# Performance work log

Hardware: AMD Instinct MI355X
Metric: run time of the kernel (lower is better)

The kernel has to match this reference:

```python
import jax, jax.numpy as jnp
import numpy as np


def setup_inputs() -> dict:
    key = jax.random.key(0)
    k1, k2 = jax.random.split(key)
    B, N, M, D = 8, 8192, 8192, 3
    gts = jax.random.normal(k1, (B, N, D), dtype=jnp.float32)
    preds = jax.random.normal(k2, (B, M, D), dtype=jnp.float32)
    return {"gts": gts, "preds": preds}


def reference(gts, preds):
    # Chamfer distance (pytorch3d defaults): squared L2, mean over points,
    # mean over batch, sum of both directions.
    x2 = jnp.sum(gts * gts, axis=-1)          # [B, N]
    y2 = jnp.sum(preds * preds, axis=-1)      # [B, M]
    xy = jnp.einsum('bnd,bmd->bnm', gts, preds)  # [B, N, M]
    d2 = x2[:, :, None] + y2[:, None, :] - 2.0 * xy
    d2 = jnp.maximum(d2, 0.0)  # guard tiny negative values from cancellation
    cham_x = jnp.mean(jnp.min(d2, axis=2))  # x -> nearest y, mean over N then B
    cham_y = jnp.mean(jnp.min(d2, axis=1))  # y -> nearest x, mean over M then B
    return cham_x + cham_y
```

## Files before the change

kernel.cpp:

```cpp
#include <hip/hip_runtime.h>
#include <hip/hip_bf16.h>
#include <math.h>


#define BLOCK 256
#define WAVES 4
#define QPW 64
#define NCHUNK 2
#define SREF 512
#define STAGE_BYTES (SREF * 32)
#define IPS (SREF / 64)

typedef short short8 __attribute__((ext_vector_type(8)));
typedef float f32x16 __attribute__((ext_vector_type(16)));
typedef unsigned int u32;
typedef __attribute__((address_space(1))) const u32 gu32;
typedef __attribute__((address_space(3))) u32 lu32;

__device__ __forceinline__ unsigned int bf16hi(float f) {
    __hip_bfloat16 h = __float2bfloat16(f);
    return (unsigned int)*reinterpret_cast<unsigned short*>(&h);
}
__device__ __forceinline__ float bf16f(unsigned int u) {
    unsigned short us = (unsigned short)u;
    __hip_bfloat16 h;
    *reinterpret_cast<unsigned short*>(&h) = us;
    return __bfloat162float(h);
}

__device__ __forceinline__ f32x16 mfma_bf16_z(short8 a, short8 b) {
    f32x16 d;
    asm volatile("v_mfma_f32_32x32x16_bf16 %0, %1, %2, 0"
                 : "=&v"(d) : "v"(a), "v"(b));
    return d;
}
__device__ __forceinline__ void mfma_fence4(f32x16& a, f32x16& b, f32x16& c, f32x16& d) {
    asm volatile("s_nop 7\n\ts_nop 7" : "+v"(a), "+v"(b), "+v"(c), "+v"(d));
}

__device__ __forceinline__ void gload_lds16(const void* g, void* l) {
    __builtin_amdgcn_global_load_lds((gu32*)g, (lu32*)l, 16, 0, 0);
}

__global__ void prep_kernel(const float* __restrict__ gts, const float* __restrict__ preds,
                            int nG, int nP, uint4* __restrict__ recQ,
                            unsigned char* __restrict__ recB, float* __restrict__ q2,
                            float* out) {
    const int idx = blockIdx.x * blockDim.x + threadIdx.x;
    if (idx == 0) out[0] = 0.0f;
    if (idx >= nG + nP) return;
    const float* src;
    unsigned char* rb;
    if (idx < nG) {
        src = gts + 3 * (size_t)idx;
        rb  = recB + (size_t)(idx >> 5) * 1024 + (size_t)(idx & 31) * 16;
    } else {
        const int j = idx - nG;
        src = preds + 3 * (size_t)j;
        rb  = recB + (size_t)nG * 32 + (size_t)(j >> 5) * 1024 + (size_t)(j & 31) * 16;
    }
    const float x = src[0], y = src[1], z = src[2];
    const float n2 = x * x + y * y + z * z;
    const float w = -0.5f * n2;
    q2[idx] = n2;
    const unsigned int xh = bf16hi(x), yh = bf16hi(y), zh = bf16hi(z), wh = bf16hi(w);
    const unsigned int xl = bf16hi(x - bf16f(xh));
    const unsigned int yl = bf16hi(y - bf16f(yh));
    const unsigned int zl = bf16hi(z - bf16f(zh));
    const unsigned int wl = bf16hi(w - bf16f(wh));
    const unsigned int hx = xh | (yh << 16), hz = zh | (wh << 16);
    const unsigned int lx = xl | (yl << 16), lz = zl | (wl << 16);
    recQ[idx] = make_uint4(hx, hz, lx, lz);
    *(uint4*)(rb)       = make_uint4(hx, hz, hx, hz);
    *(uint4*)(rb + 512) = make_uint4(lx, lz, 0u, 0u);
}

__global__ void __launch_bounds__(BLOCK, 4)
nn_kernel(const uint4* __restrict__ recQ, const unsigned char* __restrict__ recB,
          float* __restrict__ kpart, int N, int M, int B) {
    const int z = blockIdx.z;
    const bool dirX = (z < B);
    const int b = dirX ? z : z - B;
    const int NQ = dirX ? N : M;
    const int NR = dirX ? M : N;
    const uint4* Qr = recQ + (dirX ? 0 : (size_t)B * N) + (size_t)b * NQ;
    const int chunk = NR / NCHUNK;
    const unsigned char* Rb = recB + (dirX ? (size_t)B * N * 32 : 0)
                              + ((size_t)b * NR + (size_t)blockIdx.y * chunk) * 32;
    const int nGP = B * (N + M);
    float* outK = kpart + (size_t)blockIdx.y * nGP + (dirX ? 0 : B * N) + (size_t)b * NQ;

    const int tid = threadIdx.x;
    const int lane = tid & 63;
    const int wave = tid >> 6;
    const int m = lane & 31;
    const unsigned int loMask = (lane >= 32) ? 0u : 0xFFFFFFFFu;
    const int qBase = (blockIdx.x * WAVES + wave) * QPW;

    const uint4 q0 = Qr[qBase + m];
    const uint4 q1 = Qr[qBase + 32 + m];
    union { uint4 v; short8 s; } a;
    a.v.x = q0.x;
    a.v.y = (q0.y & 0xFFFFu) | 0x3F800000u;
    a.v.z = q0.z & loMask;
    a.v.w = q0.w & 0xFFFFu & loMask;
    const short8 A0 = a.s;
    a.v.x = q1.x;
    a.v.y = (q1.y & 0xFFFFu) | 0x3F800000u;
    a.v.z = q1.z & loMask;
    a.v.w = q1.w & 0xFFFFu & loMask;
    const short8 A1 = a.s;

    f32x16 k0, k1;
    #pragma unroll
    for (int r = 0; r < 16; ++r) { k0[r] = -INFINITY; k1[r] = -INFINITY; }

    __shared__ __align__(16) unsigned char smem[WAVES * 64 * 36 * 4];

    const unsigned char* gsrc = Rb + (size_t)wave * 4096 + (size_t)lane * 16;
    unsigned char* lbase = smem + wave * 4096;
    auto stage_issue = [&](int s) {
        const unsigned char* g = gsrc + (size_t)s * STAGE_BYTES;
        unsigned char* l = lbase + ((s & 1) * STAGE_BYTES);
        #pragma unroll
        for (int k2 = 0; k2 < 4; ++k2)
            gload_lds16(g + k2 * 1024, l + k2 * 1024);
    };

    const int nStages = chunk / SREF;
    stage_issue(0);
    __syncthreads();

    #pragma unroll 1
    for (int s = 0; s < nStages; ++s) {
        if (s + 1 < nStages) stage_issue(s + 1);
        const unsigned char* tb = smem + ((s & 1) * STAGE_BYTES) + lane * 16;
        #pragma unroll
        for (int i = 0; i < IPS; ++i) {
            const short8 b0 = *(const short8*)(tb + i * 2048);
            const short8 b1 = *(const short8*)(tb + i * 2048 + 1024);

            f32x16 c0 = mfma_bf16_z(A0, b0);
            f32x16 c1 = mfma_bf16_z(A0, b1);
            f32x16 c2 = mfma_bf16_z(A1, b0);
            f32x16 c3 = mfma_bf16_z(A1, b1);
            mfma_fence4(c0, c1, c2, c3);
            #pragma unroll
            for (int r = 0; r < 16; ++r)
                k0[r] = fmaxf(fmaxf(c0[r], c1[r]), k0[r]);
            #pragma unroll
            for (int r = 0; r < 16; ++r)
                k1[r] = fmaxf(fmaxf(c2[r], c3[r]), k1[r]);
        }
        __syncthreads();
    }

    float (*sT)[64][36] = (float (*)[64][36])smem;
    #pragma unroll
    for (int r = 0; r < 16; ++r) {
        const int row = (r & 3) + 8 * (r >> 2) + 4 * (lane >> 5);
        sT[wave][row][m]      = k0[r];
        sT[wave][32 + row][m] = k1[r];
    }
    const float4* rowp = (const float4*)&sT[wave][lane][0];
    float4 m01 = rowp[0];
    #pragma unroll
    for (int kk = 1; kk < 8; ++kk) {
        const float4 t = rowp[kk];
        m01.x = fmaxf(m01.x, t.x); m01.y = fmaxf(m01.y, t.y);
        m01.z = fmaxf(m01.z, t.z); m01.w = fmaxf(m01.w, t.w);
    }
    const float cmax = fmaxf(fmaxf(m01.x, m01.y), fmaxf(m01.z, m01.w));
    outK[qBase + lane] = cmax;
}

__global__ void __launch_bounds__(BLOCK)
reduce_kernel(const float* __restrict__ kpart, const float* __restrict__ q2,
              int nG, int nP, float invx, float invy, float* __restrict__ out) {
    const int total = nG + nP;
    float local = 0.0f;
    for (int idx = blockIdx.x * blockDim.x + threadIdx.x; idx < total;
         idx += gridDim.x * blockDim.x) {
        const float c = fmaxf(kpart[idx], kpart[total + idx]);
        const float inv = (idx < nG) ? invx : invy;
        local += fmaxf(q2[idx] - 2.0f * c, 0.0f) * inv;
    }
    __shared__ float waveSums[BLOCK / 64];
    float v = local;
    #pragma unroll
    for (int off = 32; off; off >>= 1) v += __shfl_xor(v, off);
    if ((threadIdx.x & 63) == 0) waveSums[threadIdx.x >> 6] = v;
    __syncthreads();
    if (threadIdx.x == 0) {
        float s = 0.0f;
        #pragma unroll
        for (int w = 0; w < BLOCK / 64; ++w) s += waveSums[w];
        atomicAdd(out, s);
    }
}

extern "C" void kernel_launch(void* const* d_in, const int* in_sizes, int n_in,
                              void* d_out, int out_size, void* d_ws, size_t ws_size,
                              hipStream_t stream) {
    const float* gts   = (const float*)d_in[0];
    const float* preds = (const float*)d_in[1];
    float* out = (float*)d_out;

    const int B = 8;
    const int N = in_sizes[0] / (B * 3);
    const int M = in_sizes[1] / (B * 3);
    const int nG = B * N, nP = B * M;

    uint4* recQ = (uint4*)d_ws;
    unsigned char* recB = (unsigned char*)(recQ + nG + nP);
    float* kpart = (float*)(recB + (size_t)(nG + nP) * 32);
    float* q2    = kpart + (size_t)NCHUNK * (nG + nP);

    prep_kernel<<<(nG + nP + BLOCK - 1) / BLOCK, BLOCK, 0, stream>>>(
        gts, preds, nG, nP, recQ, recB, q2, out);

    dim3 grid(N / (WAVES * QPW), NCHUNK, 2 * B);
    nn_kernel<<<grid, BLOCK, 0, stream>>>(recQ, recB, kpart, N, M, B);

    reduce_kernel<<<256, BLOCK, 0, stream>>>(
        kpart, q2, nG, nP, 1.0f / (float)nG, 1.0f / (float)nP, out);
}
```

Measured before the change: 99.49 us.

## Software-pipeline MFMA with max-folding using double-buffered accumulator sets

Result: no change. 98.17 us (-1.3%).

```diff
diff --git a/kernel.cpp b/kernel.cpp
--- a/kernel.cpp
+++ b/kernel.cpp
@@ -17,6 +17,8 @@
 typedef __attribute__((address_space(1))) const u32 gu32;
 typedef __attribute__((address_space(3))) u32 lu32;
 
+#define SB() __builtin_amdgcn_sched_barrier(0)
+
 __device__ __forceinline__ unsigned int bf16hi(float f) {
     __hip_bfloat16 h = __float2bfloat16(f);
     return (unsigned int)*reinterpret_cast<unsigned short*>(&h);
@@ -34,12 +36,22 @@
                  : "=&v"(d) : "v"(a), "v"(b));
     return d;
 }
+
 __device__ __forceinline__ void mfma_fence4(f32x16& a, f32x16& b, f32x16& c, f32x16& d) {
-    asm volatile("s_nop 7\n\ts_nop 7" : "+v"(a), "+v"(b), "+v"(c), "+v"(d));
+    asm volatile("s_nop 7" : "+v"(a), "+v"(b), "+v"(c), "+v"(d));
 }
 
 __device__ __forceinline__ void gload_lds16(const void* g, void* l) {
     __builtin_amdgcn_global_load_lds((gu32*)g, (lu32*)l, 16, 0, 0);
+}
+
+__device__ __forceinline__ void fold4(const f32x16& x, const f32x16& y,
+                                      const f32x16& z, const f32x16& w,
+                                      f32x16& k0, f32x16& k1) {
+    #pragma unroll
+    for (int r = 0; r < 16; ++r) k0[r] = fmaxf(fmaxf(x[r], y[r]), k0[r]);
+    #pragma unroll
+    for (int r = 0; r < 16; ++r) k1[r] = fmaxf(fmaxf(z[r], w[r]), k1[r]);
 }
 
 __global__ void prep_kernel(const float* __restrict__ gts, const float* __restrict__ preds,
@@ -75,7 +87,7 @@
     *(uint4*)(rb + 512) = make_uint4(lx, lz, 0u, 0u);
 }
 
-__global__ void __launch_bounds__(BLOCK, 4)
+__global__ void __launch_bounds__(BLOCK, 2)
 nn_kernel(const uint4* __restrict__ recQ, const unsigned char* __restrict__ recB,
           float* __restrict__ kpart, int N, int M, int B) {
     const int z = blockIdx.z;
@@ -115,6 +127,13 @@
     #pragma unroll
     for (int r = 0; r < 16; ++r) { k0[r] = -INFINITY; k1[r] = -INFINITY; }
 
+    f32x16 cA0, cA1, cA2, cA3, cB0, cB1, cB2, cB3;
+    #pragma unroll
+    for (int r = 0; r < 16; ++r) {
+        cB0[r] = -INFINITY; cB1[r] = -INFINITY;
+        cB2[r] = -INFINITY; cB3[r] = -INFINITY;
+    }
+
     __shared__ __align__(16) unsigned char smem[WAVES * 64 * 36 * 4];
 
     const unsigned char* gsrc = Rb + (size_t)wave * 4096 + (size_t)lane * 16;
@@ -135,25 +154,39 @@
     for (int s = 0; s < nStages; ++s) {
         if (s + 1 < nStages) stage_issue(s + 1);
         const unsigned char* tb = smem + ((s & 1) * STAGE_BYTES) + lane * 16;
+        short8 b0 = *(const short8*)(tb);
+        short8 b1 = *(const short8*)(tb + 1024);
         #pragma unroll
-        for (int i = 0; i < IPS; ++i) {
-            const short8 b0 = *(const short8*)(tb + i * 2048);
-            const short8 b1 = *(const short8*)(tb + i * 2048 + 1024);
-
-            f32x16 c0 = mfma_bf16_z(A0, b0);
-            f32x16 c1 = mfma_bf16_z(A0, b1);
-            f32x16 c2 = mfma_bf16_z(A1, b0);
-            f32x16 c3 = mfma_bf16_z(A1, b1);
-            mfma_fence4(c0, c1, c2, c3);
-            #pragma unroll
-            for (int r = 0; r < 16; ++r)
-                k0[r] = fmaxf(fmaxf(c0[r], c1[r]), k0[r]);
-            #pragma unroll
-            for (int r = 0; r < 16; ++r)
-                k1[r] = fmaxf(fmaxf(c2[r], c3[r]), k1[r]);
+        for (int ii = 0; ii < IPS / 2; ++ii) {
+            const short8 n0 = *(const short8*)(tb + (2 * ii + 1) * 2048);
+            const short8 n1 = *(const short8*)(tb + (2 * ii + 1) * 2048 + 1024);
+            cA0 = mfma_bf16_z(A0, b0);
+            cA1 = mfma_bf16_z(A0, b1);
+            cA2 = mfma_bf16_z(A1, b0);
+            cA3 = mfma_bf16_z(A1, b1);
+            SB();
+            mfma_fence4(cB0, cB1, cB2, cB3);
+            fold4(cB0, cB1, cB2, cB3, k0, k1);
+
+            short8 m0 = b0, m1 = b1;
+            if (2 * ii + 2 < IPS) {
+                m0 = *(const short8*)(tb + (2 * ii + 2) * 2048);
+                m1 = *(const short8*)(tb + (2 * ii + 2) * 2048 + 1024);
+            }
+            cB0 = mfma_bf16_z(A0, n0);
+            cB1 = mfma_bf16_z(A0, n1);
+            cB2 = mfma_bf16_z(A1, n0);
+            cB3 = mfma_bf16_z(A1, n1);
+            SB();
+            mfma_fence4(cA0, cA1, cA2, cA3);
+            fold4(cA0, cA1, cA2, cA3, k0, k1);
+
+            b0 = m0; b1 = m1;
         }
         __syncthreads();
     }
+    mfma_fence4(cB0, cB1, cB2, cB3);
+    fold4(cB0, cB1, cB2, cB3, k0, k1);
 
     float (*sT)[64][36] = (float (*)[64][36])smem;
     #pragma unroll
```
